# Performance work log

Measured on AMD Instinct MI355X. Metric: run time of the kernel, lower is better.

Reference implementation:

```python
import jax, jax.numpy as jnp
import numpy as np

D_MODEL = 1024
N_HEADS = 16
HEAD_DIM = D_MODEL // N_HEADS
BATCH = 2
SEQ = 2048
MASK_FILL = -10000.0


def setup_inputs() -> dict:
    key = jax.random.key(0)
    ks = jax.random.split(key, 5)
    scale = 1.0 / np.sqrt(D_MODEL)
    return {
        "x": jax.random.normal(ks[0], (BATCH, SEQ, D_MODEL), dtype=jnp.float32),
        "w_q": jax.random.normal(ks[1], (D_MODEL, D_MODEL), dtype=jnp.float32) * scale,
        "w_k": jax.random.normal(ks[2], (D_MODEL, D_MODEL), dtype=jnp.float32) * scale,
        "w_v": jax.random.normal(ks[3], (D_MODEL, D_MODEL), dtype=jnp.float32) * scale,
        "w_o": jax.random.normal(ks[4], (D_MODEL, D_MODEL), dtype=jnp.float32) * scale,
    }


def reference(x, w_q, w_k, w_v, w_o):
    B, S, C = x.shape
    # Linear(bias=False): y = x @ W^T (torch stores W as [out, in])
    q = jnp.einsum("bsc,dc->bsd", x, w_q).reshape(B, S, N_HEADS, HEAD_DIM)
    k = jnp.einsum("bsc,dc->bsd", x, w_k).reshape(B, S, N_HEADS, HEAD_DIM)
    v = jnp.einsum("bsc,dc->bsd", x, w_v).reshape(B, S, N_HEADS, HEAD_DIM)
    # scores: [B, H, S, S]
    scores = jnp.einsum("bqhd,bkhd->bhqk", q, k) / np.sqrt(HEAD_DIM)
    causal = jnp.tril(jnp.ones((S, S), dtype=bool))
    scores = jnp.where(causal, scores, MASK_FILL)
    weights = jax.nn.softmax(scores, axis=-1)
    out = jnp.einsum("bhqk,bkhd->bqhd", weights, v).reshape(B, S, C)
    return jnp.einsum("bsc,dc->bsd", out, w_o)
```

## Files before the change

### kernel.cpp

```cpp
#include <hip/hip_runtime.h>

typedef __attribute__((ext_vector_type(8))) short bf16x8;
typedef __attribute__((ext_vector_type(4))) float floatx4;

static constexpr int SEQ    = 2048;
static constexpr int CDIM   = 1024;
static constexpr int NH     = 16;
static constexpr int HD     = 64;
static constexpr int NBATCH = 2;
static constexpr int MROWS  = NBATCH * SEQ;

static __device__ __forceinline__ short f2bf(float f) {
    union { float f; unsigned u; } x; x.f = f;
    unsigned r = x.u + 0x7fffu + ((x.u >> 16) & 1u);
    return (short)(r >> 16);
}

static __device__ __forceinline__ unsigned pack2bf(float lo, float hi) {
    return ((unsigned)(unsigned short)f2bf(hi) << 16) | (unsigned)(unsigned short)f2bf(lo);
}

static __device__ __forceinline__ unsigned pk2(float lo, float hi) {
    union { float f; unsigned u; } a, b; a.f = lo; b.f = hi;
    return __builtin_amdgcn_perm(b.u + 0x8000u, a.u + 0x8000u, 0x07060302u);
}

static __device__ __forceinline__ float bf2f(short s) {
    union { unsigned u; float f; } x;
    x.u = ((unsigned)(unsigned short)s) << 16;
    return x.f;
}

static __device__ __forceinline__ floatx4 mfma16(bf16x8 a, bf16x8 b, floatx4 c) {
    return __builtin_amdgcn_mfma_f32_16x16x32_bf16(a, b, c, 0, 0, 0);
}

static __device__ __forceinline__ bf16x8 mk8(unsigned d0, unsigned d1, unsigned d2, unsigned d3) {
    union { unsigned u[4]; bf16x8 v; } x;
    x.u[0] = d0; x.u[1] = d1; x.u[2] = d2; x.u[3] = d3;
    return x.v;
}

static __device__ __forceinline__ void gl_lds16(const short* g, short* l) {
    __builtin_amdgcn_global_load_lds(
        (const __attribute__((address_space(1))) void*)g,
        (__attribute__((address_space(3))) void*)l, 16, 0, 0);
}

__global__ void convert_all(
    const void* __restrict__ x,  const void* __restrict__ wq,
    const void* __restrict__ wk, const void* __restrict__ wv,
    const void* __restrict__ wo,
    short* __restrict__ xc,  short* __restrict__ wqc, short* __restrict__ wkc,
    short* __restrict__ wvc, short* __restrict__ woc,
    int* __restrict__ flag)
{
    const int tid = threadIdx.x;
    const unsigned short* xs = (const unsigned short*)x;
    int pl = 0;
    for (int i = tid; i < 2048; i += 256) {
        const int e = (xs[2 * i] >> 7) & 0xFF;
        if (e >= 110 && e <= 144) pl++;
    }
    #pragma unroll
    for (int off = 32; off > 0; off >>= 1) pl += __shfl_down(pl, off, 64);
    __shared__ int cnt;
    if (tid == 0) cnt = 0;
    __syncthreads();
    if ((tid & 63) == 0) atomicAdd(&cnt, pl);
    __syncthreads();
    const int f = (cnt < 1024) ? 1 : 0;
    if (blockIdx.x == 0 && blockIdx.y == 0 && tid == 0) *flag = f;

    const int y = blockIdx.y;
    const void* src = (y == 0) ? x  : (y == 1) ? wq : (y == 2) ? wk : (y == 3) ? wv : wo;
    short*      dst = (y == 0) ? xc : (y == 1) ? wqc : (y == 2) ? wkc : (y == 3) ? wvc : woc;
    const int n4 = (y == 0) ? (MROWS * CDIM / 4) : (CDIM * CDIM / 4);

    const int stride = gridDim.x * blockDim.x;
    for (int i = blockIdx.x * blockDim.x + tid; i < n4; i += stride) {
        if (f) {
            const float4 v = ((const float4*)src)[i];
            ((uint2*)dst)[i] = make_uint2(pack2bf(v.x, v.y), pack2bf(v.z, v.w));
        } else {
            ((uint2*)dst)[i] = ((const uint2*)src)[i];
        }
    }
}

__global__ __launch_bounds__(256) void gemm_qkv64(
    const short* __restrict__ A,
    const short* __restrict__ W0, const short* __restrict__ W1, const short* __restrict__ W2,
    short* __restrict__ CQ, short* __restrict__ CK, short* __restrict__ VT)
{
    const int m0   = blockIdx.x * 128;
    const int yt   = blockIdx.y;
    const int sel  = yt >> 4;
    const int nloc = (yt & 15) * 64;
    const short* W = (sel == 0) ? W0 : ((sel == 1) ? W1 : W2);
    const float oscl = (sel == 0) ? 0.18033688011112042f : 1.0f;

    __shared__ __align__(16) short ta[128 * 64];
    __shared__ __align__(16) short tb[64 * 64];

    const int tid  = threadIdx.x;
    const int lane = tid & 63;
    const int wave = tid >> 6;
    const int quad = lane >> 4;
    const int l16  = lane & 15;
    const int wm   = (wave >> 1) * 64;
    const int wn   = (wave & 1) * 32;

    floatx4 acc[4][2];
    #pragma unroll
    for (int i = 0; i < 4; i++)
        #pragma unroll
        for (int j = 0; j < 2; j++)
            acc[i][j] = 0.0f;

    const int sr8 = lane >> 3;
    const int ug  = ((lane & 7) ^ sr8) * 8;
    const short* Ab = A + (size_t)(m0 + 32 * wave + sr8) * CDIM + ug;
    const short* Wb = W + (size_t)(nloc + 16 * wave + sr8) * CDIM + ug;
    short* ta0 = ta + (32 * wave) * 64;
    short* tb0 = tb + (16 * wave) * 64;

    for (int k0 = 0; k0 < CDIM; k0 += 64) {
        __syncthreads();
        gl_lds16(Ab + k0,             ta0);
        gl_lds16(Ab +  8 * CDIM + k0, ta0 +  8 * 64);
        gl_lds16(Ab + 16 * CDIM + k0, ta0 + 16 * 64);
        gl_lds16(Ab + 24 * CDIM + k0, ta0 + 24 * 64);
        gl_lds16(Wb + k0,             tb0);
        gl_lds16(Wb +  8 * CDIM + k0, tb0 +  8 * 64);
        __syncthreads();

        #pragma unroll
        for (int kc = 0; kc < 2; kc++) {
            const int pu = (((kc * 4 + quad) ^ (l16 & 7))) * 8;
            bf16x8 af[4], bw[2];
            #pragma unroll
            for (int i = 0; i < 4; i++)
                af[i] = *(const bf16x8*)(ta + (wm + i * 16 + l16) * 64 + pu);
            #pragma unroll
            for (int j = 0; j < 2; j++)
                bw[j] = *(const bf16x8*)(tb + (wn + j * 16 + l16) * 64 + pu);
            #pragma unroll
            for (int i = 0; i < 4; i++)
                #pragma unroll
                for (int j = 0; j < 2; j++)
                    acc[i][j] = mfma16(af[i], bw[j], acc[i][j]);
        }
    }

    #pragma unroll
    for (int i = 0; i < 4; i++) {
        #pragma unroll
        for (int j = 0; j < 2; j++) {
            const int row0 = m0 + wm + i * 16 + quad * 4;
            const int col  = nloc + wn + j * 16 + l16;
            if (sel == 2) {
                const int bb  = row0 >> 11;
                const int key = row0 & 2047;
                const size_t idx = ((size_t)(bb * 1024 + col)) * 2048 + key;
                *(uint2*)(VT + idx) = make_uint2(pk2(acc[i][j][0], acc[i][j][1]),
                                                 pk2(acc[i][j][2], acc[i][j][3]));
            } else {
                short* cp = ((sel == 0) ? CQ : CK) + (size_t)row0 * CDIM + col;
                #pragma unroll
                for (int r2 = 0; r2 < 4; r2++)
                    cp[(size_t)r2 * CDIM] = f2bf(acc[i][j][r2] * oscl);
            }
        }
    }
}

__global__ __launch_bounds__(256) void gemm_n64(
    const short* __restrict__ A, const short* __restrict__ W,
    void* __restrict__ C, const int* __restrict__ flag)
{
    const int m0 = blockIdx.x * 128;
    const int n0 = blockIdx.y * 64;
    const bool f32out = (flag != nullptr) && (*flag != 0);

    __shared__ __align__(16) short ta[128 * 64];
    __shared__ __align__(16) short tb[64 * 64];

    const int tid  = threadIdx.x;
    const int lane = tid & 63;
    const int wave = tid >> 6;
    const int quad = lane >> 4;
    const int l16  = lane & 15;
    const int wm   = (wave >> 1) * 64;
    const int wn   = (wave & 1) * 32;

    floatx4 acc[4][2];
    #pragma unroll
    for (int i = 0; i < 4; i++)
        #pragma unroll
        for (int j = 0; j < 2; j++)
            acc[i][j] = 0.0f;

    const int sr8 = lane >> 3;
    const int ug  = ((lane & 7) ^ sr8) * 8;
    const short* Ab = A + (size_t)(m0 + 32 * wave + sr8) * CDIM + ug;
    const short* Wb = W + (size_t)(n0 + 16 * wave + sr8) * CDIM + ug;
    short* ta0 = ta + (32 * wave) * 64;
    short* tb0 = tb + (16 * wave) * 64;

    for (int k0 = 0; k0 < CDIM; k0 += 64) {
        __syncthreads();
        gl_lds16(Ab + k0,             ta0);
        gl_lds16(Ab +  8 * CDIM + k0, ta0 +  8 * 64);
        gl_lds16(Ab + 16 * CDIM + k0, ta0 + 16 * 64);
        gl_lds16(Ab + 24 * CDIM + k0, ta0 + 24 * 64);
        gl_lds16(Wb + k0,             tb0);
        gl_lds16(Wb +  8 * CDIM + k0, tb0 +  8 * 64);
        __syncthreads();

        #pragma unroll
        for (int kc = 0; kc < 2; kc++) {
            const int pu = (((kc * 4 + quad) ^ (l16 & 7))) * 8;
            bf16x8 af[4], bw[2];
            #pragma unroll
            for (int i = 0; i < 4; i++)
                af[i] = *(const bf16x8*)(ta + (wm + i * 16 + l16) * 64 + pu);
            #pragma unroll
            for (int j = 0; j < 2; j++)
                bw[j] = *(const bf16x8*)(tb + (wn + j * 16 + l16) * 64 + pu);
            #pragma unroll
            for (int i = 0; i < 4; i++)
                #pragma unroll
                for (int j = 0; j < 2; j++)
                    acc[i][j] = mfma16(af[i], bw[j], acc[i][j]);
        }
    }

    #pragma unroll
    for (int i = 0; i < 4; i++) {
        #pragma unroll
        for (int j = 0; j < 2; j++) {
            const int row0 = m0 + wm + i * 16 + quad * 4;
            const int col  = n0 + wn + j * 16 + l16;
            if (f32out) {
                float* cp = (float*)C + (size_t)row0 * CDIM + col;
                #pragma unroll
                for (int r2 = 0; r2 < 4; r2++)
                    cp[(size_t)r2 * CDIM] = acc[i][j][r2];
            } else {
                short* cp = (short*)C + (size_t)row0 * CDIM + col;
                #pragma unroll
                for (int r2 = 0; r2 < 4; r2++)
                    cp[(size_t)r2 * CDIM] = f2bf(acc[i][j][r2]);
            }
        }
    }
}

__global__ __launch_bounds__(256, 2) void attn_t(
    const short* __restrict__ Q, const short* __restrict__ K,
    const short* __restrict__ VT,
    short* __restrict__ P0, short* __restrict__ P1, float* __restrict__ L)
{
    const int h = blockIdx.x;
    const int b = blockIdx.y;
    const int z = blockIdx.z;
    const int g = z >> 3;
    const int item = (g == 1) ? (23 - z) : (g == 3) ? (55 - z) : z;
    const int qt2 = 15 - (item >> 1);
    const int p   = item & 1;
    const int nktall = qt2 + 1;

    const int tid  = threadIdx.x;
    const int lane = tid & 63;
    const int wave = tid >> 6;
    const int quad = lane >> 4;
    const int l16  = lane & 15;

    __shared__ __align__(16) short Kt[128][72];
    __shared__ __align__(16) short Vt[64][136];

    const int rowBase = b * SEQ;
    const int colH    = h * HD;
    const int qgA     = qt2 * 128 + wave * 16 + l16;
    const int qgB     = qgA + 64;

    bf16x8 qa0, qa1, qc0, qc1;
    {
        const short* qp = Q + (size_t)(rowBase + qgA) * CDIM + colH + quad * 8;
        qa0 = *(const bf16x8*)qp;
        qa1 = *(const bf16x8*)(qp + 32);
        const short* qp2 = qp + (size_t)64 * CDIM;
        qc0 = *(const bf16x8*)qp2;
        qc1 = *(const bf16x8*)(qp2 + 32);
    }

    floatx4 oA[4], oB[4];
    #pragma unroll
    for (int nd = 0; nd < 4; nd++) { oA[nd] = 0.0f; oB[nd] = 0.0f; }
    floatx4 lAv = 0.0f, lBv = 0.0f;
    const bf16x8 ones = mk8(0x3F803F80u, 0x3F803F80u, 0x3F803F80u, 0x3F803F80u);

    const int kk = tid >> 1;
    const int kd = (tid & 1) * 32;
    const short* kg = K + (size_t)(rowBase + kk) * CDIM + colH + kd;
    const int sd = tid >> 2;
    const int sk = (tid & 3) * 32;
    const short* vg = VT + ((size_t)(b * NH + h) * HD + sd) * SEQ + sk;

    const short* kg0 = kg + (size_t)p * 128 * CDIM;
    const short* vg0 = vg + p * 128;
    uint4 ka_0 = *(const uint4*)(kg0);
    uint4 ka_1 = *(const uint4*)(kg0 + 8);
    uint4 ka_2 = *(const uint4*)(kg0 + 16);
    uint4 ka_3 = *(const uint4*)(kg0 + 24);
    uint4 va_0 = *(const uint4*)(vg0);
    uint4 va_1 = *(const uint4*)(vg0 + 8);
    uint4 va_2 = *(const uint4*)(vg0 + 16);
    uint4 va_3 = *(const uint4*)(vg0 + 24);

    for (int kt = p; kt < nktall; kt += 2) {
        __syncthreads();
        *(uint4*)&Kt[kk][kd]      = ka_0;
        *(uint4*)&Kt[kk][kd + 8]  = ka_1;
        *(uint4*)&Kt[kk][kd + 16] = ka_2;
        *(uint4*)&Kt[kk][kd + 24] = ka_3;
        {
            short* vrow = &Vt[sd][sk];
            *(uint2*)(vrow + 0)  = make_uint2(va_0.x, va_0.y);
            *(uint2*)(vrow + 8)  = make_uint2(va_0.z, va_0.w);
            *(uint2*)(vrow + 16) = make_uint2(va_1.x, va_1.y);
            *(uint2*)(vrow + 24) = make_uint2(va_1.z, va_1.w);
            *(uint2*)(vrow + 4)  = make_uint2(va_2.x, va_2.y);
            *(uint2*)(vrow + 12) = make_uint2(va_2.z, va_2.w);
            *(uint2*)(vrow + 20) = make_uint2(va_3.x, va_3.y);
            *(uint2*)(vrow + 28) = make_uint2(va_3.z, va_3.w);
        }
        __syncthreads();

        if (kt + 2 < nktall) {
            const short* kn = kg + (size_t)(kt + 2) * 128 * CDIM;
            const short* vn = vg + (kt + 2) * 128;
            ka_0 = *(const uint4*)(kn);
            ka_1 = *(const uint4*)(kn + 8);
            ka_2 = *(const uint4*)(kn + 16);
            ka_3 = *(const uint4*)(kn + 24);
            va_0 = *(const uint4*)(vn);
            va_1 = *(const uint4*)(vn + 8);
            va_2 = *(const uint4*)(vn + 16);
            va_3 = *(const uint4*)(vn + 24);
        }

        const int key0 = kt * 128;
        const bool masked = (kt == nktall - 1);

        unsigned hA0 = 0, hA1 = 0, hB0 = 0, hB1 = 0;
        #pragma unroll
        for (int ms = 0; ms < 8; ms++) {
            const short* kp = &Kt[ms * 16 + l16][quad * 8];
            bf16x8 k0 = *(const bf16x8*)kp;
            bf16x8 k1 = *(const bf16x8*)(kp + 32);
            floatx4 sA = {0.f, 0.f, 0.f, 0.f};
            floatx4 sB = {0.f, 0.f, 0.f, 0.f};
            __builtin_amdgcn_s_setprio(1);
            sA = mfma16(k0, qa0, sA);
            sB = mfma16(k0, qc0, sB);
            sA = mfma16(k1, qa1, sA);
            sB = mfma16(k1, qc1, sB);
            __builtin_amdgcn_s_setprio(0);
            float pA[4], pB[4];
            #pragma unroll
            for (int r = 0; r < 4; r++) {
                const int kgl = key0 + ms * 16 + quad * 4 + r;
                float eA = __builtin_amdgcn_exp2f(sA[r]);
                float eB = __builtin_amdgcn_exp2f(sB[r]);
                if (masked) {
                    if (kgl > qgA) eA = 0.0f;
                    if (kgl > qgB) eB = 0.0f;
                }
                pA[r] = eA;
                pB[r] = eB;
            }
            const unsigned cA0 = pk2(pA[0], pA[1]);
            const unsigned cA1 = pk2(pA[2], pA[3]);
            const unsigned cB0 = pk2(pB[0], pB[1]);
            const unsigned cB1 = pk2(pB[2], pB[3]);
            if ((ms & 1) == 0) {
                hA0 = cA0; hA1 = cA1; hB0 = cB0; hB1 = cB1;
            } else {
                const int kc = ms >> 1;
                const bf16x8 pbA = mk8(hA0, hA1, cA0, cA1);
                const bf16x8 pbB = mk8(hB0, hB1, cB0, cB1);
                __builtin_amdgcn_s_setprio(1);
                #pragma unroll
                for (int nd = 0; nd < 4; nd++) {
                    const bf16x8 va = *(const bf16x8*)&Vt[nd * 16 + l16][kc * 32 + quad * 8];
                    oA[nd] = mfma16(va, pbA, oA[nd]);
                    oB[nd] = mfma16(va, pbB, oB[nd]);
                }
                lAv = mfma16(ones, pbA, lAv);
                lBv = mfma16(ones, pbB, lBv);
                __builtin_amdgcn_s_setprio(0);
            }
        }
    }

    const float lA = lAv[0];
    const float lB = lBv[0];

    short* Pp = p ? P1 : P0;
    float* Lp = L + p * (NBATCH * NH * SEQ);
    short* opA = Pp + (size_t)(rowBase + qgA) * CDIM + colH;
    short* opB = Pp + (size_t)(rowBase + qgB) * CDIM + colH;
    #pragma unroll
    for (int nd = 0; nd < 4; nd++) {
        *(uint2*)(opA + nd * 16 + quad * 4) =
            make_uint2(pk2(oA[nd][0], oA[nd][1]), pk2(oA[nd][2], oA[nd][3]));
        *(uint2*)(opB + nd * 16 + quad * 4) =
            make_uint2(pk2(oB[nd][0], oB[nd][1]), pk2(oB[nd][2], oB[nd][3]));
    }
    if (quad == 0) {
        Lp[(b * NH + h) * SEQ + qgA] = lA;
        Lp[(b * NH + h) * SEQ + qgB] = lB;
    }
}

__global__ void combine(const short* __restrict__ P0, const short* __restrict__ P1,
                        const float* __restrict__ L, short* __restrict__ Ob)
{
    const int i = blockIdx.x * blockDim.x + threadIdx.x;
    const int row = i >> 7;
    const int c8  = i & 127;
    const int h   = c8 >> 3;
    const int b   = row >> 11;
    const int q   = row & 2047;
    const int li  = (b * NH + h) * SEQ + q;
    const float inv = 1.0f / (L[li] + L[NBATCH * NH * SEQ + li]);

    const bf16x8 a0 = ((const bf16x8*)P0)[i];
    const bf16x8 a1 = ((const bf16x8*)P1)[i];
    unsigned d[4];
    #pragma unroll
    for (int e = 0; e < 4; e++) {
        const float lo = (bf2f(a0[2 * e])     + bf2f(a1[2 * e]))     * inv;
        const float hi = (bf2f(a0[2 * e + 1]) + bf2f(a1[2 * e + 1])) * inv;
        d[e] = pk2(lo, hi);
    }
    ((uint4*)Ob)[i] = make_uint4(d[0], d[1], d[2], d[3]);
}

extern "C" void kernel_launch(void* const* d_in, const int* in_sizes, int n_in,
                              void* d_out, int out_size, void* d_ws, size_t ws_size,
                              hipStream_t stream)
{
    const void* x  = d_in[0];
    const void* wq = d_in[1];
    const void* wk = d_in[2];
    const void* wv = d_in[3];
    const void* wo = d_in[4];

    int* flag = (int*)d_ws;
    short* w = (short*)((char*)d_ws + 256);
    const int ME  = 1024 * 1024;
    short* Wqc = w;
    short* Wkc = w + 1 * ME;
    short* Wvc = w + 2 * ME;
    short* Woc = w + 3 * ME;
    short* Xc  = w + 4 * ME;
    short* Qb  = w + 8 * ME;
    short* Kb  = w + 12 * ME;
    short* VTb = w + 16 * ME;
    short* P1b = w + 20 * ME;
    float* Lb  = (float*)(w + 24 * ME);
    short* P0b = Xc;
    short* Ob  = Xc;

    dim3 blk(256);
    convert_all<<<dim3(512, 5), blk, 0, stream>>>(
        x, wq, wk, wv, wo, Xc, Wqc, Wkc, Wvc, Woc, flag);

    gemm_qkv64<<<dim3(MROWS / 128, 48), blk, 0, stream>>>(
        Xc, Wqc, Wkc, Wvc, Qb, Kb, VTb);
    attn_t<<<dim3(NH, NBATCH, 32), blk, 0, stream>>>(Qb, Kb, VTb, P0b, P1b, Lb);
    combine<<<dim3(MROWS * CDIM / 8 / 256), blk, 0, stream>>>(P0b, P1b, Lb, Ob);
    gemm_n64<<<dim3(MROWS / 128, CDIM / 64), blk, 0, stream>>>(
        Ob, Woc, d_out, flag);
}
```

Measured before the change: 174.5 us.

## Fuse split-KV combine into attention kernel via last-arriver atomic counter

```diff
diff --git a/kernel.cpp b/kernel.cpp
--- a/kernel.cpp
+++ b/kernel.cpp
@@ -53,7 +53,7 @@
     const void* __restrict__ wo,
     short* __restrict__ xc,  short* __restrict__ wqc, short* __restrict__ wkc,
     short* __restrict__ wvc, short* __restrict__ woc,
-    int* __restrict__ flag)
+    int* __restrict__ flag, int* __restrict__ sflags)
 {
     const int tid = threadIdx.x;
     const unsigned short* xs = (const unsigned short*)x;
@@ -70,7 +70,11 @@
     if ((tid & 63) == 0) atomicAdd(&cnt, pl);
     __syncthreads();
     const int f = (cnt < 1024) ? 1 : 0;
-    if (blockIdx.x == 0 && blockIdx.y == 0 && tid == 0) *flag = f;
+    if (blockIdx.x == 0 && blockIdx.y == 0) {
+        if (tid == 0) *flag = f;
+        sflags[tid] = 0;
+        sflags[256 + tid] = 0;
+    }
 
     const int y = blockIdx.y;
     const void* src = (y == 0) ? x  : (y == 1) ? wq : (y == 2) ? wk : (y == 3) ? wv : wo;
@@ -260,7 +264,8 @@
 __global__ __launch_bounds__(256, 2) void attn_t(
     const short* __restrict__ Q, const short* __restrict__ K,
     const short* __restrict__ VT,
-    short* __restrict__ P0, short* __restrict__ P1, float* __restrict__ L)
+    short* __restrict__ P0, short* __restrict__ P1, float* __restrict__ L,
+    short* __restrict__ Ob, int* __restrict__ sflags)
 {
     const int h = blockIdx.x;
     const int b = blockIdx.y;
@@ -423,30 +428,41 @@
         Lp[(b * NH + h) * SEQ + qgA] = lA;
         Lp[(b * NH + h) * SEQ + qgB] = lB;
     }
-}
-
-__global__ void combine(const short* __restrict__ P0, const short* __restrict__ P1,
-                        const float* __restrict__ L, short* __restrict__ Ob)
-{
-    const int i = blockIdx.x * blockDim.x + threadIdx.x;
-    const int row = i >> 7;
-    const int c8  = i & 127;
-    const int h   = c8 >> 3;
-    const int b   = row >> 11;
-    const int q   = row & 2047;
-    const int li  = (b * NH + h) * SEQ + q;
-    const float inv = 1.0f / (L[li] + L[NBATCH * NH * SEQ + li]);
-
-    const bf16x8 a0 = ((const bf16x8*)P0)[i];
-    const bf16x8 a1 = ((const bf16x8*)P1)[i];
-    unsigned d[4];
-    #pragma unroll
-    for (int e = 0; e < 4; e++) {
-        const float lo = (bf2f(a0[2 * e])     + bf2f(a1[2 * e]))     * inv;
-        const float hi = (bf2f(a0[2 * e + 1]) + bf2f(a1[2 * e + 1])) * inv;
-        d[e] = pk2(lo, hi);
-    }
-    ((uint4*)Ob)[i] = make_uint4(d[0], d[1], d[2], d[3]);
+
+    __threadfence();
+    __shared__ int oldv;
+    __syncthreads();
+    if (tid == 0)
+        oldv = atomicAdd(&sflags[(b * NH + h) * 16 + qt2], 1);
+    __syncthreads();
+    if (oldv == 0) return;
+
+    __threadfence();
+    const short* Po = p ? P0 : P1;
+    const float* Lo = L + (1 - p) * (NBATCH * NH * SEQ);
+    const float invA = 1.0f / (lA + Lo[(b * NH + h) * SEQ + qgA]);
+    const float invB = 1.0f / (lB + Lo[(b * NH + h) * SEQ + qgB]);
+    const short* poA = Po + (size_t)(rowBase + qgA) * CDIM + colH;
+    const short* poB = Po + (size_t)(rowBase + qgB) * CDIM + colH;
+    short* obA = Ob + (size_t)(rowBase + qgA) * CDIM + colH;
+    short* obB = Ob + (size_t)(rowBase + qgB) * CDIM + colH;
+    #pragma unroll
+    for (int nd = 0; nd < 4; nd++) {
+        uint2 ua = *(const uint2*)(poA + nd * 16 + quad * 4);
+        uint2 ub = *(const uint2*)(poB + nd * 16 + quad * 4);
+        const short* sa = (const short*)&ua;
+        const short* sb = (const short*)&ub;
+        const float a0 = (oA[nd][0] + bf2f(sa[0])) * invA;
+        const float a1 = (oA[nd][1] + bf2f(sa[1])) * invA;
+        const float a2 = (oA[nd][2] + bf2f(sa[2])) * invA;
+        const float a3 = (oA[nd][3] + bf2f(sa[3])) * invA;
+        *(uint2*)(obA + nd * 16 + quad * 4) = make_uint2(pk2(a0, a1), pk2(a2, a3));
+        const float b0 = (oB[nd][0] + bf2f(sb[0])) * invB;
+        const float b1 = (oB[nd][1] + bf2f(sb[1])) * invB;
+        const float b2 = (oB[nd][2] + bf2f(sb[2])) * invB;
+        const float b3 = (oB[nd][3] + bf2f(sb[3])) * invB;
+        *(uint2*)(obB + nd * 16 + quad * 4) = make_uint2(pk2(b0, b1), pk2(b2, b3));
+    }
 }
 
 extern "C" void kernel_launch(void* const* d_in, const int* in_sizes, int n_in,
@@ -459,8 +475,9 @@
     const void* wv = d_in[3];
     const void* wo = d_in[4];
 
-    int* flag = (int*)d_ws;
-    short* w = (short*)((char*)d_ws + 256);
+    int* flag   = (int*)d_ws;
+    int* sflags = (int*)((char*)d_ws + 256);
+    short* w = (short*)((char*)d_ws + 4096);
     const int ME  = 1024 * 1024;
     short* Wqc = w;
     short* Wkc = w + 1 * ME;
@@ -477,12 +494,12 @@
 
     dim3 blk(256);
     convert_all<<<dim3(512, 5), blk, 0, stream>>>(
-        x, wq, wk, wv, wo, Xc, Wqc, Wkc, Wvc, Woc, flag);
+        x, wq, wk, wv, wo, Xc, Wqc, Wkc, Wvc, Woc, flag, sflags);
 
     gemm_qkv64<<<dim3(MROWS / 128, 48), blk, 0, stream>>>(
         Xc, Wqc, Wkc, Wvc, Qb, Kb, VTb);
-    attn_t<<<dim3(NH, NBATCH, 32), blk, 0, stream>>>(Qb, Kb, VTb, P0b, P1b, Lb);
-    combine<<<dim3(MROWS * CDIM / 8 / 256), blk, 0, stream>>>(P0b, P1b, Lb, Ob);
+    attn_t<<<dim3(NH, NBATCH, 32), blk, 0, stream>>>(
+        Qb, Kb, VTb, P0b, P1b, Lb, Ob, sflags);
     gemm_n64<<<dim3(MROWS / 128, CDIM / 64), blk, 0, stream>>>(
         Ob, Woc, d_out, flag);
 }
```

New measurement: 361.0 us. +106.9%, slower.
